# Kernel optimization log

Hardware: AMD Instinct MI355X
Metric: run time of the kernel (lower is better)

## Reference

```python
import jax, jax.numpy as jnp
import numpy as np

HID = 64


def setup_inputs() -> dict:
    key = jax.random.key(0)
    k = jax.random.split(key, 7)
    B, T = 4096, 8192
    x = jax.random.normal(k[0], (B, T, 1), dtype=jnp.float32)
    # Kaiming-uniform-ish init scale; exact values irrelevant for correctness baseline
    W_in = jax.random.normal(k[1], (1, HID), dtype=jnp.float32) * 0.5
    b_in = jax.random.normal(k[2], (HID,), dtype=jnp.float32) * 0.1
    W_s = jax.random.normal(k[3], (HID, HID), dtype=jnp.float32) * (1.0 / np.sqrt(HID))
    b_s = jax.random.normal(k[4], (HID,), dtype=jnp.float32) * 0.1
    W_out = jax.random.normal(k[5], (HID, 1), dtype=jnp.float32) * (1.0 / np.sqrt(HID))
    b_out = jax.random.normal(k[6], (1,), dtype=jnp.float32) * 0.1
    return {"x": x, "W_in": W_in, "b_in": b_in, "W_s": W_s, "b_s": b_s,
            "W_out": W_out, "b_out": b_out}


def reference(x, W_in, b_in, W_s, b_s, W_out, b_out):
    B, T, _ = x.shape
    xt = jnp.swapaxes(x, 0, 1)  # [T, B, 1] -> scan over time

    def step(h, x_t):
        # input_proj on [B,1] -> [B,HID]; tiny GEMM per step (the recurrence is sequential)
        inp = x_t @ W_in + b_in
        h = jax.nn.gelu(h @ W_s + b_s + inp, approximate=False)  # torch GELU = exact erf
        return h, None

    h0 = jnp.zeros((B, HID), dtype=x.dtype)
    h_final, _ = jax.lax.scan(step, h0, xt)
    return h_final @ W_out + b_out  # [B, 1]
```

## Files before the change

### kernel.cpp

```cpp
#include <hip/hip_runtime.h>
#include <cstdint>
#include <cstddef>

#define HID 64
#define RPG 16
#define ROWU 144
#define XSTR 68

typedef short bf16x8 __attribute__((ext_vector_type(8)));
typedef float f32x4 __attribute__((ext_vector_type(4)));
typedef float f32x2 __attribute__((ext_vector_type(2)));

__device__ __forceinline__ f32x2 c2(float v) { f32x2 r = {v, v}; return r; }

__device__ __forceinline__ f32x2 fast_gelu2(f32x2 z) {
    const f32x2 u = z * 0.70710678118654752f;
    const f32x2 a = __builtin_elementwise_abs(u);
    const f32x2 d = __builtin_elementwise_fma(c2(0.3275911f), a, c2(1.0f));
    f32x2 t;
    t.x = __builtin_amdgcn_rcpf(d.x);
    t.y = __builtin_amdgcn_rcpf(d.y);
    const f32x2 s = u * 1.20112240878645f;
    f32x2 e;
    e.x = __builtin_amdgcn_exp2f(-(s.x * s.x));
    e.y = __builtin_amdgcn_exp2f(-(s.y * s.y));
    f32x2 p = c2(1.061405429f);
    p = __builtin_elementwise_fma(p, t, c2(-1.453152027f));
    p = __builtin_elementwise_fma(p, t, c2( 1.421413741f));
    p = __builtin_elementwise_fma(p, t, c2(-0.284496736f));
    p = __builtin_elementwise_fma(p, t, c2( 0.254829592f));
    p = p * t;
    f32x2 er = __builtin_elementwise_fma(-p, e, c2(1.0f));
    er = __builtin_elementwise_copysign(er, u);
    const f32x2 zh = z * 0.5f;
    return __builtin_elementwise_fma(zh, er, zh);
}

__device__ __forceinline__ ushort bf16_hi(float f) {
    return (ushort)(__float_as_uint(f) >> 16);
}
__device__ __forceinline__ float bf16_f(ushort u) {
    return __uint_as_float(((unsigned)u) << 16);
}

#define PKHI(b_, a_) __builtin_amdgcn_perm((b_), (a_), 0x07060302u)

#define STEP(RA0, RA1, WHI, WLO, XB, E0, E1) { \
    const bf16x8 Hhi0 = *reinterpret_cast<const bf16x8*>(RA0); \
    const bf16x8 Hlo0 = *reinterpret_cast<const bf16x8*>((RA0) + 64); \
    const bf16x8 Hhi1 = *reinterpret_cast<const bf16x8*>(RA1); \
    const bf16x8 Hlo1 = *reinterpret_cast<const bf16x8*>((RA1) + 64); \
    const f32x2 biv = __builtin_elementwise_fma(c2(XB), winv, cbv); \
    f32x4 ci = {0.f, 0.f, 0.f, 0.f}; \
    ci[E0] = biv.x; \
    ci[E1] = biv.y; \
    const f32x4 zz = {0.f, 0.f, 0.f, 0.f}; \
    f32x4 ahh = __builtin_amdgcn_mfma_f32_16x16x32_bf16(Whi0, Hhi0, zz, 0, 0, 0); \
    f32x4 ac1 = __builtin_amdgcn_mfma_f32_16x16x32_bf16(Whi0, Hlo0, ci, 0, 0, 0); \
    f32x4 ac2 = __builtin_amdgcn_mfma_f32_16x16x32_bf16(Wlo0, Hhi0, zz, 0, 0, 0); \
    ahh = __builtin_amdgcn_mfma_f32_16x16x32_bf16(Whi1, Hhi1, ahh, 0, 0, 0); \
    ac1 = __builtin_amdgcn_mfma_f32_16x16x32_bf16(Whi1, Hlo1, ac1, 0, 0, 0); \
    ac2 = __builtin_amdgcn_mfma_f32_16x16x32_bf16(Wlo1, Hhi1, ac2, 0, 0, 0); \
    f32x2 pa, pb, pc; \
    pa.x = ahh[E0]; pa.y = ahh[E1]; \
    pb.x = ac1[E0]; pb.y = ac1[E1]; \
    pc.x = ac2[E0]; pc.y = ac2[E1]; \
    const f32x2 zv = (pa + pb) + pc; \
    const f32x2 hv = fast_gelu2(zv); \
    const unsigned hb0 = __float_as_uint(hv.x), hb1 = __float_as_uint(hv.y); \
    *(WHI) = PKHI(hb1, hb0); \
    const f32x2 htr = { __uint_as_float(hb0 & 0xffff0000u), \
                        __uint_as_float(hb1 & 0xffff0000u) }; \
    const f32x2 lv = hv - htr; \
    *(WLO) = PKHI(__float_as_uint(lv.y), __float_as_uint(lv.x)); \
    __syncthreads(); }

#define MAINLOOP(E0, E1) { \
    f32x2 winv, cbv; \
    winv.x = W_in[cq + E0]; winv.y = W_in[cq + E1]; \
    cbv.x  = b_in[cq + E0] + b_s[cq + E0]; \
    cbv.y  = b_in[cq + E1] + b_s[cq + E1]; \
    for (int tc = 0; tc < nch; ++tc) { \
         \
         \
        asm volatile("" : "+v"(Whi0), "+v"(Whi1), "+v"(Wlo0), "+v"(Wlo1)); \
        const size_t tg = (size_t)tc * 64; \
        { \
            const int row = tid >> 5;         \
            const int ch  = tid & 31;         \
            const float2 xg = *reinterpret_cast<const float2*>( \
                &x[(size_t)(bA + row) * (size_t)T + tg + ch * 2]); \
            *reinterpret_cast<float2*>(&xlds[row][ch * 2]) = xg; \
        } \
        __syncthreads(); \
        _Pragma("unroll 1") \
        for (int t4 = 0; t4 < 16; ++t4) { \
            const f32x4 xq = *reinterpret_cast<const f32x4*>(&xlds[rr][t4 * 4]); \
            STEP(rA0, rA1, whiB, wloB, xq[0], E0, E1) \
            STEP(rB0, rB1, whiA, wloA, xq[1], E0, E1) \
            STEP(rA0, rA1, whiB, wloB, xq[2], E0, E1) \
            STEP(rB0, rB1, whiA, wloA, xq[3], E0, E1) \
        } \
    } }

__global__ __launch_bounds__(512, 2)
void ssm_kernel(const float* __restrict__ x,
                const float* __restrict__ W_in,
                const float* __restrict__ b_in,
                const float* __restrict__ W_s,
                const float* __restrict__ b_s,
                const float* __restrict__ W_out,
                const float* __restrict__ b_out,
                float* __restrict__ out,
                int B, int T) {
    __shared__ ushort hlds[2][RPG * ROWU];
    __shared__ float  xlds[RPG][XSTR];

    const int tid  = threadIdx.x;
    const int ww   = tid >> 6;
    const int g    = ww & 3;
    const int hf   = ww >> 2;
    const int lane = tid & 63;
    const int q    = lane >> 4;
    const int rr   = lane & 15;
    const int bA   = blockIdx.x * RPG;
    const int cq   = 16 * g + 4 * q;

    if (bA >= B) return;

    bf16x8 Whi0, Whi1, Wlo0, Wlo1;
    const int wcol = 16 * g + rr;
#pragma unroll
    for (int e = 0; e < 8; ++e) {
        {   const float wf = W_s[(8 * q + e) * HID + wcol];
            const ushort hi = bf16_hi(wf);
            Whi0[e] = (short)hi;
            Wlo0[e] = (short)bf16_hi(wf - bf16_f(hi)); }
        {   const float wf = W_s[(32 + 8 * q + e) * HID + wcol];
            const ushort hi = bf16_hi(wf);
            Whi1[e] = (short)hi;
            Wlo1[e] = (short)bf16_hi(wf - bf16_f(hi)); }
    }
    asm volatile("" : "+v"(Whi0), "+v"(Whi1), "+v"(Wlo0), "+v"(Wlo1));

    {
        ushort* p = &hlds[0][0];
        for (int i = tid; i < 2 * RPG * ROWU; i += 512) p[i] = 0;
    }

    const int sx = (rr & 7) ^ ((rr >> 3) * 5);

    const ushort* const rA0 = &hlds[0][rr * ROWU + 8 * (q ^ sx)];
    const ushort* const rA1 = &hlds[0][rr * ROWU + 8 * ((q ^ 4) ^ sx)];
    const ushort* const rB0 = &hlds[1][rr * ROWU + 8 * (q ^ sx)];
    const ushort* const rB1 = &hlds[1][rr * ROWU + 8 * ((q ^ 4) ^ sx)];

    const int c0  = cq + 2 * hf;
    const int wl  = c0 >> 3;
    const int win_idx = rr * ROWU + 8 * (wl ^ sx) + (c0 & 7);
    unsigned* const whiA = reinterpret_cast<unsigned*>(&hlds[0][win_idx]);
    unsigned* const wloA = reinterpret_cast<unsigned*>(&hlds[0][win_idx + 64]);
    unsigned* const whiB = reinterpret_cast<unsigned*>(&hlds[1][win_idx]);
    unsigned* const wloB = reinterpret_cast<unsigned*>(&hlds[1][win_idx + 64]);

    const int nch = T >> 6;

    if (hf == 0) { MAINLOOP(0, 1) } else { MAINLOOP(2, 3) }

    if (ww == 0) {
        const int r  = lane >> 2;
        const int p4 = lane & 3;
        const int sxr = (r & 7) ^ ((r >> 3) * 5);
        float s = 0.f;
#pragma unroll
        for (int half = 0; half < 2; ++half) {
            const int slot = 2 * p4 + half;
            const ushort* hp = &hlds[0][r * ROWU + 8 * (slot ^ sxr)];
            const ushort* lp = hp + 64;
#pragma unroll
            for (int j = 0; j < 8; ++j) {
                const float hv = bf16_f(hp[j]) + bf16_f(lp[j]);
                s = __builtin_fmaf(hv, W_out[8 * slot + j], s);
            }
        }
        s += __shfl_xor(s, 1, 64);
        s += __shfl_xor(s, 2, 64);
        if (p4 == 0) out[bA + r] = s + b_out[0];
    }
}

extern "C" void kernel_launch(void* const* d_in, const int* in_sizes, int n_in,
                              void* d_out, int out_size, void* d_ws, size_t ws_size,
                              hipStream_t stream) {
    const float* x     = (const float*)d_in[0];
    const float* W_in  = (const float*)d_in[1];
    const float* b_in  = (const float*)d_in[2];
    const float* W_s   = (const float*)d_in[3];
    const float* b_s   = (const float*)d_in[4];
    const float* W_out = (const float*)d_in[5];
    const float* b_out = (const float*)d_in[6];
    float* out = (float*)d_out;

    const int B = out_size;
    const int T = in_sizes[0] / B;

    const int blocks = B / RPG;
    ssm_kernel<<<blocks, 512, 0, stream>>>(
        x, W_in, b_in, W_s, b_s, W_out, b_out, out, B, T);
}
```

Before: 2.565 ms.

## Halve rows per block and let each wave compute all four MFMA output lanes

Each block now handles 8 batch rows with 256 threads (4 waves) instead of 16 rows with 512 threads (8 waves), giving twice as many blocks. Each wave now applies GELU and writes all four accumulator elements per lane, where before two waves split that work. The MFMA tile still spans 16 rows, so half of each tile is wasted on zero-padded rows. The aim is cheaper per-block barriers and more blocks to schedule, at the cost of doubled per-wave GELU work on the sequential critical path and doubled total MFMA work per useful row.

```diff
diff --git a/kernel.cpp b/kernel.cpp
--- a/kernel.cpp
+++ b/kernel.cpp
@@ -3,7 +3,7 @@
 #include <cstddef>
 
 #define HID 64
-#define RPG 16
+#define RPG 8
 #define ROWU 144
 #define XSTR 68
 
@@ -45,15 +45,13 @@
 
 #define PKHI(b_, a_) __builtin_amdgcn_perm((b_), (a_), 0x07060302u)
 
-#define STEP(RA0, RA1, WHI, WLO, XB, E0, E1) { \
+#define STEP(RA0, RA1, WHI, WLO, XB) { \
     const bf16x8 Hhi0 = *reinterpret_cast<const bf16x8*>(RA0); \
     const bf16x8 Hlo0 = *reinterpret_cast<const bf16x8*>((RA0) + 64); \
     const bf16x8 Hhi1 = *reinterpret_cast<const bf16x8*>(RA1); \
     const bf16x8 Hlo1 = *reinterpret_cast<const bf16x8*>((RA1) + 64); \
-    const f32x2 biv = __builtin_elementwise_fma(c2(XB), winv, cbv); \
-    f32x4 ci = {0.f, 0.f, 0.f, 0.f}; \
-    ci[E0] = biv.x; \
-    ci[E1] = biv.y; \
+    f32x4 xb4; xb4[0] = (XB); xb4[1] = (XB); xb4[2] = (XB); xb4[3] = (XB); \
+    const f32x4 ci = __builtin_elementwise_fma(xb4, winv, cbv); \
     const f32x4 zz = {0.f, 0.f, 0.f, 0.f}; \
     f32x4 ahh = __builtin_amdgcn_mfma_f32_16x16x32_bf16(Whi0, Hhi0, zz, 0, 0, 0); \
     f32x4 ac1 = __builtin_amdgcn_mfma_f32_16x16x32_bf16(Whi0, Hlo0, ci, 0, 0, 0); \
@@ -61,49 +59,27 @@
     ahh = __builtin_amdgcn_mfma_f32_16x16x32_bf16(Whi1, Hhi1, ahh, 0, 0, 0); \
     ac1 = __builtin_amdgcn_mfma_f32_16x16x32_bf16(Whi1, Hlo1, ac1, 0, 0, 0); \
     ac2 = __builtin_amdgcn_mfma_f32_16x16x32_bf16(Wlo1, Hhi1, ac2, 0, 0, 0); \
-    f32x2 pa, pb, pc; \
-    pa.x = ahh[E0]; pa.y = ahh[E1]; \
-    pb.x = ac1[E0]; pb.y = ac1[E1]; \
-    pc.x = ac2[E0]; pc.y = ac2[E1]; \
-    const f32x2 zv = (pa + pb) + pc; \
-    const f32x2 hv = fast_gelu2(zv); \
-    const unsigned hb0 = __float_as_uint(hv.x), hb1 = __float_as_uint(hv.y); \
-    *(WHI) = PKHI(hb1, hb0); \
-    const f32x2 htr = { __uint_as_float(hb0 & 0xffff0000u), \
-                        __uint_as_float(hb1 & 0xffff0000u) }; \
-    const f32x2 lv = hv - htr; \
-    *(WLO) = PKHI(__float_as_uint(lv.y), __float_as_uint(lv.x)); \
+    const f32x4 zv = (ahh + ac1) + ac2; \
+    f32x2 z01; z01.x = zv[0]; z01.y = zv[1]; \
+    f32x2 z23; z23.x = zv[2]; z23.y = zv[3]; \
+    const f32x2 h01 = fast_gelu2(z01); \
+    const f32x2 h23 = fast_gelu2(z23); \
+    const unsigned hb0 = __float_as_uint(h01.x), hb1 = __float_as_uint(h01.y); \
+    const unsigned hb2 = __float_as_uint(h23.x), hb3 = __float_as_uint(h23.y); \
+    uint2 hpk; hpk.x = PKHI(hb1, hb0); hpk.y = PKHI(hb3, hb2); \
+    const f32x2 tr01 = { __uint_as_float(hb0 & 0xffff0000u), \
+                         __uint_as_float(hb1 & 0xffff0000u) }; \
+    const f32x2 tr23 = { __uint_as_float(hb2 & 0xffff0000u), \
+                         __uint_as_float(hb3 & 0xffff0000u) }; \
+    const f32x2 l01 = h01 - tr01; \
+    const f32x2 l23 = h23 - tr23; \
+    uint2 lpk; \
+    lpk.x = PKHI(__float_as_uint(l01.y), __float_as_uint(l01.x)); \
+    lpk.y = PKHI(__float_as_uint(l23.y), __float_as_uint(l23.x)); \
+    if (rr < RPG) { *(WHI) = hpk; *(WLO) = lpk; } \
     __syncthreads(); }
 
-#define MAINLOOP(E0, E1) { \
-    f32x2 winv, cbv; \
-    winv.x = W_in[cq + E0]; winv.y = W_in[cq + E1]; \
-    cbv.x  = b_in[cq + E0] + b_s[cq + E0]; \
-    cbv.y  = b_in[cq + E1] + b_s[cq + E1]; \
-    for (int tc = 0; tc < nch; ++tc) { \
-         \
-         \
-        asm volatile("" : "+v"(Whi0), "+v"(Whi1), "+v"(Wlo0), "+v"(Wlo1)); \
-        const size_t tg = (size_t)tc * 64; \
-        { \
-            const int row = tid >> 5;         \
-            const int ch  = tid & 31;         \
-            const float2 xg = *reinterpret_cast<const float2*>( \
-                &x[(size_t)(bA + row) * (size_t)T + tg + ch * 2]); \
-            *reinterpret_cast<float2*>(&xlds[row][ch * 2]) = xg; \
-        } \
-        __syncthreads(); \
-        _Pragma("unroll 1") \
-        for (int t4 = 0; t4 < 16; ++t4) { \
-            const f32x4 xq = *reinterpret_cast<const f32x4*>(&xlds[rr][t4 * 4]); \
-            STEP(rA0, rA1, whiB, wloB, xq[0], E0, E1) \
-            STEP(rB0, rB1, whiA, wloA, xq[1], E0, E1) \
-            STEP(rA0, rA1, whiB, wloB, xq[2], E0, E1) \
-            STEP(rB0, rB1, whiA, wloA, xq[3], E0, E1) \
-        } \
-    } }
-
-__global__ __launch_bounds__(512, 2)
+__global__ __launch_bounds__(256, 2)
 void ssm_kernel(const float* __restrict__ x,
                 const float* __restrict__ W_in,
                 const float* __restrict__ b_in,
@@ -113,13 +89,11 @@
                 const float* __restrict__ b_out,
                 float* __restrict__ out,
                 int B, int T) {
-    __shared__ ushort hlds[2][RPG * ROWU];
-    __shared__ float  xlds[RPG][XSTR];
+    __shared__ ushort hlds[2][16 * ROWU];
+    __shared__ float  xlds[16][XSTR];
 
     const int tid  = threadIdx.x;
-    const int ww   = tid >> 6;
-    const int g    = ww & 3;
-    const int hf   = ww >> 2;
+    const int g    = tid >> 6;
     const int lane = tid & 63;
     const int q    = lane >> 4;
     const int rr   = lane & 15;
@@ -143,9 +117,18 @@
     }
     asm volatile("" : "+v"(Whi0), "+v"(Whi1), "+v"(Wlo0), "+v"(Wlo1));
 
+    f32x4 winv, cbv;
+#pragma unroll
+    for (int e = 0; e < 4; ++e) {
+        winv[e] = W_in[cq + e];
+        cbv[e]  = b_in[cq + e] + b_s[cq + e];
+    }
+
     {
         ushort* p = &hlds[0][0];
-        for (int i = tid; i < 2 * RPG * ROWU; i += 512) p[i] = 0;
+        for (int i = tid; i < 2 * 16 * ROWU; i += 256) p[i] = 0;
+        float* xp = &xlds[0][0];
+        for (int i = tid; i < 16 * XSTR; i += 256) xp[i] = 0.f;
     }
 
     const int sx = (rr & 7) ^ ((rr >> 3) * 5);
@@ -155,37 +138,57 @@
     const ushort* const rB0 = &hlds[1][rr * ROWU + 8 * (q ^ sx)];
     const ushort* const rB1 = &hlds[1][rr * ROWU + 8 * ((q ^ 4) ^ sx)];
 
-    const int c0  = cq + 2 * hf;
-    const int wl  = c0 >> 3;
-    const int win_idx = rr * ROWU + 8 * (wl ^ sx) + (c0 & 7);
-    unsigned* const whiA = reinterpret_cast<unsigned*>(&hlds[0][win_idx]);
-    unsigned* const wloA = reinterpret_cast<unsigned*>(&hlds[0][win_idx + 64]);
-    unsigned* const whiB = reinterpret_cast<unsigned*>(&hlds[1][win_idx]);
-    unsigned* const wloB = reinterpret_cast<unsigned*>(&hlds[1][win_idx + 64]);
+    const int wl = cq >> 3;
+    const int win_idx = rr * ROWU + 8 * (wl ^ sx) + (cq & 7);
+    uint2* const whiA = reinterpret_cast<uint2*>(&hlds[0][win_idx]);
+    uint2* const wloA = reinterpret_cast<uint2*>(&hlds[0][win_idx + 64]);
+    uint2* const whiB = reinterpret_cast<uint2*>(&hlds[1][win_idx]);
+    uint2* const wloB = reinterpret_cast<uint2*>(&hlds[1][win_idx + 64]);
 
     const int nch = T >> 6;
 
-    if (hf == 0) { MAINLOOP(0, 1) } else { MAINLOOP(2, 3) }
-
-    if (ww == 0) {
+    for (int tc = 0; tc < nch; ++tc) {
+        const size_t tg = (size_t)tc * 64;
+        {
+            const int row = tid >> 5;
+            const int ch  = tid & 31;
+            const float2 xg = *reinterpret_cast<const float2*>(
+                &x[(size_t)(bA + row) * (size_t)T + tg + ch * 2]);
+            *reinterpret_cast<float2*>(&xlds[row][ch * 2]) = xg;
+        }
+        __syncthreads();
+
+#pragma unroll 1
+        for (int t4 = 0; t4 < 16; ++t4) {
+            const f32x4 xq = *reinterpret_cast<const f32x4*>(&xlds[rr][t4 * 4]);
+            STEP(rA0, rA1, whiB, wloB, xq[0])
+            STEP(rB0, rB1, whiA, wloA, xq[1])
+            STEP(rA0, rA1, whiB, wloB, xq[2])
+            STEP(rB0, rB1, whiA, wloA, xq[3])
+        }
+    }
+
+    if (g == 0) {
         const int r  = lane >> 2;
         const int p4 = lane & 3;
-        const int sxr = (r & 7) ^ ((r >> 3) * 5);
-        float s = 0.f;
-#pragma unroll
-        for (int half = 0; half < 2; ++half) {
-            const int slot = 2 * p4 + half;
-            const ushort* hp = &hlds[0][r * ROWU + 8 * (slot ^ sxr)];
-            const ushort* lp = hp + 64;
-#pragma unroll
-            for (int j = 0; j < 8; ++j) {
-                const float hv = bf16_f(hp[j]) + bf16_f(lp[j]);
-                s = __builtin_fmaf(hv, W_out[8 * slot + j], s);
+        if (r < RPG) {
+            const int sxr = (r & 7) ^ ((r >> 3) * 5);
+            float s = 0.f;
+#pragma unroll
+            for (int half = 0; half < 2; ++half) {
+                const int slot = 2 * p4 + half;
+                const ushort* hp = &hlds[0][r * ROWU + 8 * (slot ^ sxr)];
+                const ushort* lp = hp + 64;
+#pragma unroll
+                for (int j = 0; j < 8; ++j) {
+                    const float hv = bf16_f(hp[j]) + bf16_f(lp[j]);
+                    s = __builtin_fmaf(hv, W_out[8 * slot + j], s);
+                }
             }
+            s += __shfl_xor(s, 1, 64);
+            s += __shfl_xor(s, 2, 64);
+            if (p4 == 0) out[bA + r] = s + b_out[0];
         }
-        s += __shfl_xor(s, 1, 64);
-        s += __shfl_xor(s, 2, 64);
-        if (p4 == 0) out[bA + r] = s + b_out[0];
     }
 }
 
@@ -205,6 +208,6 @@
     const int T = in_sizes[0] / B;
 
     const int blocks = B / RPG;
-    ssm_kernel<<<blocks, 512, 0, stream>>>(
+    ssm_kernel<<<blocks, 256, 0, stream>>>(
         x, W_in, b_in, W_s, b_s, W_out, b_out, out, B, T);
 }
```

New measurement: 3.389 ms. 1.32x slower.
